# Kernel tuning notes

Measured on AMD Instinct MI355X. Metric: run time of the kernel, lower is better.

Reference implementation:

```python
import jax, jax.numpy as jnp
import numpy as np

DEPTH = 4
V = 4          # num_variables
B = 131072     # batch


def _level_counts(D, v):
    # n[d] = number of tree nodes whose depth attribute is d
    n = [0] * (D + 1)
    n[D] = 1
    for d in range(D, 1, -1):
        n[d - 1] = n[d] * (v + 1)   # v subformulas + 1 last_subformula
    n[0] = n[1]                      # each depth-1 node has exactly one depth-0 last
    return n


def setup_inputs() -> dict:
    key = jax.random.key(0)
    n = _level_counts(DEPTH, V)
    ks = jax.random.split(key, 2 * DEPTH + 2)
    inp = {"x": jax.random.uniform(ks[0], (B, V), jnp.float32, 0.5, 1.5)}
    # depth-0 constants (one per depth-0 node), like nn.Parameter(2*randn) but
    # scaled for numerical sanity of the deep product tree
    inp["lam0"] = jax.random.normal(ks[1], (n[0],), jnp.float32)
    for d in range(1, DEPTH + 1):
        inp[f"lam{d}"] = jax.random.normal(ks[2 * d], (n[d], V), jnp.float32)
        inp[f"pow{d}"] = 0.5 * jax.random.normal(ks[2 * d + 1], (n[d], V), jnp.float32)
    return inp


def reference(x, lam0, lam1, pow1, lam2, pow2, lam3, pow3, lam4, pow4):
    # Vectorized evaluation of the recursive tree, level by level.
    # Level d holds n_d independent NestedFormula nodes; each produces a (B,) vector.
    xt = x.T  # (V, B)
    batch = x.shape[0]
    # depth-0 nodes: constant lambda broadcast over batch
    f = jnp.broadcast_to(lam0[:, None], (lam0.shape[0], batch))  # (n0, B)
    lams = [lam1, lam2, lam3, lam4]
    pows = [pow1, pow2, pow3, pow4]
    for d in range(1, DEPTH + 1):
        lam, pw = lams[d - 1], pows[d - 1]           # (n_d, V)
        xp = xt[None, :, :] ** pw[:, :, None]        # (n_d, V, B): x_i ** power_i
        if d == 1:
            # subformula_result == 1; last subformula is the matching depth-0 node
            f = jnp.einsum('nv,nvb->nb', lam, xp) + f
        else:
            # children of node j at level d are nodes j*(V+1) .. j*(V+1)+V at level d-1:
            # first V are subformulas, last one is last_subformula
            fr = f.reshape(lam.shape[0], V + 1, batch)
            f = jnp.einsum('nv,nvb->nb', lam, xp * fr[:, :V, :]) + fr[:, V, :]
    return f[0][:, None]  # (B, 1)
```

## Files before the change

### kernel.cpp

```cpp
#include <hip/hip_runtime.h>


#define VV 4

__global__ __launch_bounds__(256) void nested_formula_kernel(
    const float4* __restrict__ x,
    const float*  __restrict__ lam0,
    const float*  __restrict__ lam1,
    const float*  __restrict__ pow1,
    const float*  __restrict__ lam2,
    const float*  __restrict__ pow2,
    const float*  __restrict__ lam3,
    const float*  __restrict__ pow3,
    const float*  __restrict__ lam4,
    const float*  __restrict__ pow4,
    float* __restrict__ out,
    int B)
{
    int b = blockIdx.x * blockDim.x + threadIdx.x;
    if (b >= B) return;

    float4 xv = x[b];
    float lx[VV] = { log2f(xv.x), log2f(xv.y), log2f(xv.z), log2f(xv.w) };

    float acc4 = 0.f, last4 = 0.f;
#pragma unroll
    for (int c3 = 0; c3 < VV + 1; ++c3) {
        float acc3 = 0.f, last3 = 0.f;
#pragma unroll
        for (int c2 = 0; c2 < VV + 1; ++c2) {
            int n2 = c3 * (VV + 1) + c2;
            float acc2 = 0.f, last2 = 0.f;
#pragma unroll
            for (int c1 = 0; c1 < VV + 1; ++c1) {
                int n1 = n2 * (VV + 1) + c1;
                float f1 = lam0[n1];
#pragma unroll
                for (int v = 0; v < VV; ++v) {
                    float xp = exp2f(pow1[n1 * VV + v] * lx[v]);
                    f1 = fmaf(lam1[n1 * VV + v], xp, f1);
                }
                if (c1 < VV) {
                    float xp = exp2f(pow2[n2 * VV + c1] * lx[c1]);
                    acc2 = fmaf(lam2[n2 * VV + c1] * xp, f1, acc2);
                } else {
                    last2 = f1;
                }
            }
            float f2 = acc2 + last2;
            if (c2 < VV) {
                float xp = exp2f(pow3[c3 * VV + c2] * lx[c2]);
                acc3 = fmaf(lam3[c3 * VV + c2] * xp, f2, acc3);
            } else {
                last3 = f2;
            }
        }
        float f3 = acc3 + last3;
        if (c3 < VV) {
            float xp = exp2f(pow4[c3] * lx[c3]);
            acc4 = fmaf(lam4[c3] * xp, f3, acc4);
        } else {
            last4 = f3;
        }
    }
    out[b] = acc4 + last4;
}

extern "C" void kernel_launch(void* const* d_in, const int* in_sizes, int n_in,
                              void* d_out, int out_size, void* d_ws, size_t ws_size,
                              hipStream_t stream) {
    const float4* x    = (const float4*)d_in[0];
    const float*  lam0 = (const float*)d_in[1];
    const float*  lam1 = (const float*)d_in[2];
    const float*  pow1 = (const float*)d_in[3];
    const float*  lam2 = (const float*)d_in[4];
    const float*  pow2 = (const float*)d_in[5];
    const float*  lam3 = (const float*)d_in[6];
    const float*  pow3 = (const float*)d_in[7];
    const float*  lam4 = (const float*)d_in[8];
    const float*  pow4 = (const float*)d_in[9];
    float* out = (float*)d_out;

    int B = in_sizes[0] / 4;
    int block = 256;
    int grid = (B + block - 1) / block;
    nested_formula_kernel<<<grid, block, 0, stream>>>(
        x, lam0, lam1, pow1, lam2, pow2, lam3, pow3, lam4, pow4, out, B);
}
```

Before: 95.92 us.

## Process four batch elements per thread and use raw hardware exp2/log intrinsics

Each thread now evaluates the formula tree for four batch elements, so every uniform load of the lam/pow parameters is reused across four elements, and the grid shrinks by four. The library log2f/exp2f calls are replaced by the AMDGPU hardware intrinsics, which skip denormal and range handling. This trades more registers per thread and fewer wavefronts for less scalar-load and instruction overhead, and accepts slightly different accuracy for edge-case inputs.

```diff
diff --git a/kernel.cpp b/kernel.cpp
--- a/kernel.cpp
+++ b/kernel.cpp
@@ -2,6 +2,7 @@
 
 
 #define VV 4
+#define E  4
 
 __global__ __launch_bounds__(256) void nested_formula_kernel(
     const float4* __restrict__ x,
@@ -17,53 +18,95 @@
     float* __restrict__ out,
     int B)
 {
-    int b = blockIdx.x * blockDim.x + threadIdx.x;
-    if (b >= B) return;
+    const int NT = gridDim.x * blockDim.x;
+    const int t  = blockIdx.x * blockDim.x + threadIdx.x;
 
-    float4 xv = x[b];
-    float lx[VV] = { log2f(xv.x), log2f(xv.y), log2f(xv.z), log2f(xv.w) };
+    float lx[E][VV];
+#pragma unroll
+    for (int e = 0; e < E; ++e) {
+        int b = t + e * NT;
+        float4 xv = (b < B) ? x[b] : make_float4(1.f, 1.f, 1.f, 1.f);
+        lx[e][0] = __builtin_amdgcn_logf(xv.x);
+        lx[e][1] = __builtin_amdgcn_logf(xv.y);
+        lx[e][2] = __builtin_amdgcn_logf(xv.z);
+        lx[e][3] = __builtin_amdgcn_logf(xv.w);
+    }
 
-    float acc4 = 0.f, last4 = 0.f;
+    float acc4[E], last4[E];
+#pragma unroll
+    for (int e = 0; e < E; ++e) { acc4[e] = 0.f; last4[e] = 0.f; }
+
 #pragma unroll
     for (int c3 = 0; c3 < VV + 1; ++c3) {
-        float acc3 = 0.f, last3 = 0.f;
+        float acc3[E], last3[E];
+#pragma unroll
+        for (int e = 0; e < E; ++e) { acc3[e] = 0.f; last3[e] = 0.f; }
+
 #pragma unroll
         for (int c2 = 0; c2 < VV + 1; ++c2) {
-            int n2 = c3 * (VV + 1) + c2;
-            float acc2 = 0.f, last2 = 0.f;
+            const int n2 = c3 * (VV + 1) + c2;
+            float acc2[E], last2[E];
+#pragma unroll
+            for (int e = 0; e < E; ++e) { acc2[e] = 0.f; last2[e] = 0.f; }
+
 #pragma unroll
             for (int c1 = 0; c1 < VV + 1; ++c1) {
-                int n1 = n2 * (VV + 1) + c1;
-                float f1 = lam0[n1];
+                const int n1 = n2 * (VV + 1) + c1;
+                float f1[E];
+                const float l0 = lam0[n1];
+#pragma unroll
+                for (int e = 0; e < E; ++e) f1[e] = l0;
 #pragma unroll
                 for (int v = 0; v < VV; ++v) {
-                    float xp = exp2f(pow1[n1 * VV + v] * lx[v]);
-                    f1 = fmaf(lam1[n1 * VV + v], xp, f1);
+                    const float p = pow1[n1 * VV + v];
+                    const float l = lam1[n1 * VV + v];
+#pragma unroll
+                    for (int e = 0; e < E; ++e)
+                        f1[e] = fmaf(l, __builtin_amdgcn_exp2f(p * lx[e][v]), f1[e]);
                 }
                 if (c1 < VV) {
-                    float xp = exp2f(pow2[n2 * VV + c1] * lx[c1]);
-                    acc2 = fmaf(lam2[n2 * VV + c1] * xp, f1, acc2);
+                    const float p = pow2[n2 * VV + c1];
+                    const float l = lam2[n2 * VV + c1];
+#pragma unroll
+                    for (int e = 0; e < E; ++e)
+                        acc2[e] = fmaf(l * __builtin_amdgcn_exp2f(p * lx[e][c1]), f1[e], acc2[e]);
                 } else {
-                    last2 = f1;
+#pragma unroll
+                    for (int e = 0; e < E; ++e) last2[e] = f1[e];
                 }
             }
-            float f2 = acc2 + last2;
+
             if (c2 < VV) {
-                float xp = exp2f(pow3[c3 * VV + c2] * lx[c2]);
-                acc3 = fmaf(lam3[c3 * VV + c2] * xp, f2, acc3);
+                const float p = pow3[c3 * VV + c2];
+                const float l = lam3[c3 * VV + c2];
+#pragma unroll
+                for (int e = 0; e < E; ++e)
+                    acc3[e] = fmaf(l * __builtin_amdgcn_exp2f(p * lx[e][c2]),
+                                   acc2[e] + last2[e], acc3[e]);
             } else {
-                last3 = f2;
+#pragma unroll
+                for (int e = 0; e < E; ++e) last3[e] = acc2[e] + last2[e];
             }
         }
-        float f3 = acc3 + last3;
+
         if (c3 < VV) {
-            float xp = exp2f(pow4[c3] * lx[c3]);
-            acc4 = fmaf(lam4[c3] * xp, f3, acc4);
+            const float p = pow4[c3];
+            const float l = lam4[c3];
+#pragma unroll
+            for (int e = 0; e < E; ++e)
+                acc4[e] = fmaf(l * __builtin_amdgcn_exp2f(p * lx[e][c3]),
+                               acc3[e] + last3[e], acc4[e]);
         } else {
-            last4 = f3;
+#pragma unroll
+            for (int e = 0; e < E; ++e) last4[e] = acc3[e] + last3[e];
         }
     }
-    out[b] = acc4 + last4;
+
+#pragma unroll
+    for (int e = 0; e < E; ++e) {
+        int b = t + e * NT;
+        if (b < B) out[b] = acc4[e] + last4[e];
+    }
 }
 
 extern "C" void kernel_launch(void* const* d_in, const int* in_sizes, int n_in,
@@ -83,7 +126,7 @@
 
     int B = in_sizes[0] / 4;
     int block = 256;
-    int grid = (B + block - 1) / block;
+    int grid = (B + block * E - 1) / (block * E);
     nested_formula_kernel<<<grid, block, 0, stream>>>(
         x, lam0, lam1, pow1, lam2, pow2, lam3, pow3, lam4, pow4, out, B);
 }
```

New measurement: 153.2 us. +59.7%, slower.

## Split formula tree across four grid rows and combine with atomic adds

Applied to the files above, without the earlier changes.

The grid gets a second dimension of four, and each row evaluates one slice of the depth-4 tree. The slices are the r-th depth-3 subtree, the r-th child of the last depth-3 node, and the r-th child of the innermost last chain. Partial results are summed into the output with atomics after a memset. Libm log2/exp2 are also replaced with the raw hardware intrinsics. This trades single-thread serial work for four times the threads plus memset and atomic traffic, and the per-row work is not evenly balanced.

```diff
diff --git a/kernel.cpp b/kernel.cpp
--- a/kernel.cpp
+++ b/kernel.cpp
@@ -3,7 +3,52 @@
 
 #define VV 4
 
-__global__ __launch_bounds__(256) void nested_formula_kernel(
+__device__ __forceinline__ float f1_eval(int n1, const float lx[VV],
+    const float* __restrict__ lam0, const float* __restrict__ lam1,
+    const float* __restrict__ pow1)
+{
+    float f = lam0[n1];
+#pragma unroll
+    for (int v = 0; v < VV; ++v)
+        f = fmaf(lam1[n1 * VV + v],
+                 __builtin_amdgcn_exp2f(pow1[n1 * VV + v] * lx[v]), f);
+    return f;
+}
+
+__device__ __forceinline__ float f2_eval(int n2, const float lx[VV],
+    const float* __restrict__ lam0, const float* __restrict__ lam1,
+    const float* __restrict__ pow1, const float* __restrict__ lam2,
+    const float* __restrict__ pow2)
+{
+    float acc = 0.f;
+#pragma unroll
+    for (int c1 = 0; c1 < VV; ++c1) {
+        float f1 = f1_eval(n2 * (VV + 1) + c1, lx, lam0, lam1, pow1);
+        acc = fmaf(lam2[n2 * VV + c1] *
+                       __builtin_amdgcn_exp2f(pow2[n2 * VV + c1] * lx[c1]),
+                   f1, acc);
+    }
+    return acc + f1_eval(n2 * (VV + 1) + VV, lx, lam0, lam1, pow1);
+}
+
+__device__ __forceinline__ float f3_eval(int n3, const float lx[VV],
+    const float* __restrict__ lam0, const float* __restrict__ lam1,
+    const float* __restrict__ pow1, const float* __restrict__ lam2,
+    const float* __restrict__ pow2, const float* __restrict__ lam3,
+    const float* __restrict__ pow3)
+{
+    float acc = 0.f;
+#pragma unroll
+    for (int c2 = 0; c2 < VV; ++c2) {
+        float f2 = f2_eval(n3 * (VV + 1) + c2, lx, lam0, lam1, pow1, lam2, pow2);
+        acc = fmaf(lam3[n3 * VV + c2] *
+                       __builtin_amdgcn_exp2f(pow3[n3 * VV + c2] * lx[c2]),
+                   f2, acc);
+    }
+    return acc + f2_eval(n3 * (VV + 1) + VV, lx, lam0, lam1, pow1, lam2, pow2);
+}
+
+__global__ __launch_bounds__(256) void nested_formula_r4(
     const float4* __restrict__ x,
     const float*  __restrict__ lam0,
     const float*  __restrict__ lam1,
@@ -17,53 +62,30 @@
     float* __restrict__ out,
     int B)
 {
-    int b = blockIdx.x * blockDim.x + threadIdx.x;
+    const int r = blockIdx.y;
+    const int b = blockIdx.x * blockDim.x + threadIdx.x;
     if (b >= B) return;
 
     float4 xv = x[b];
-    float lx[VV] = { log2f(xv.x), log2f(xv.y), log2f(xv.z), log2f(xv.w) };
+    float lx[VV] = { __builtin_amdgcn_logf(xv.x), __builtin_amdgcn_logf(xv.y),
+                     __builtin_amdgcn_logf(xv.z), __builtin_amdgcn_logf(xv.w) };
+    const float lxr = (r == 0) ? lx[0] : (r == 1) ? lx[1] : (r == 2) ? lx[2] : lx[3];
 
-    float acc4 = 0.f, last4 = 0.f;
-#pragma unroll
-    for (int c3 = 0; c3 < VV + 1; ++c3) {
-        float acc3 = 0.f, last3 = 0.f;
-#pragma unroll
-        for (int c2 = 0; c2 < VV + 1; ++c2) {
-            int n2 = c3 * (VV + 1) + c2;
-            float acc2 = 0.f, last2 = 0.f;
-#pragma unroll
-            for (int c1 = 0; c1 < VV + 1; ++c1) {
-                int n1 = n2 * (VV + 1) + c1;
-                float f1 = lam0[n1];
-#pragma unroll
-                for (int v = 0; v < VV; ++v) {
-                    float xp = exp2f(pow1[n1 * VV + v] * lx[v]);
-                    f1 = fmaf(lam1[n1 * VV + v], xp, f1);
-                }
-                if (c1 < VV) {
-                    float xp = exp2f(pow2[n2 * VV + c1] * lx[c1]);
-                    acc2 = fmaf(lam2[n2 * VV + c1] * xp, f1, acc2);
-                } else {
-                    last2 = f1;
-                }
-            }
-            float f2 = acc2 + last2;
-            if (c2 < VV) {
-                float xp = exp2f(pow3[c3 * VV + c2] * lx[c2]);
-                acc3 = fmaf(lam3[c3 * VV + c2] * xp, f2, acc3);
-            } else {
-                last3 = f2;
-            }
-        }
-        float f3 = acc3 + last3;
-        if (c3 < VV) {
-            float xp = exp2f(pow4[c3] * lx[c3]);
-            acc4 = fmaf(lam4[c3] * xp, f3, acc4);
-        } else {
-            last4 = f3;
-        }
-    }
-    out[b] = acc4 + last4;
+    float f3 = f3_eval(r, lx, lam0, lam1, pow1, lam2, pow2, lam3, pow3);
+    float partial = lam4[r] * __builtin_amdgcn_exp2f(pow4[r] * lxr) * f3;
+
+    float f2 = f2_eval(4 * (VV + 1) + r, lx, lam0, lam1, pow1, lam2, pow2);
+    partial = fmaf(lam3[4 * VV + r] * __builtin_amdgcn_exp2f(pow3[4 * VV + r] * lxr),
+                   f2, partial);
+
+    float f1 = f1_eval(24 * (VV + 1) + r, lx, lam0, lam1, pow1);
+    partial = fmaf(lam2[24 * VV + r] * __builtin_amdgcn_exp2f(pow2[24 * VV + r] * lxr),
+                   f1, partial);
+
+    if (r == 0)
+        partial += f1_eval(24 * (VV + 1) + VV, lx, lam0, lam1, pow1);
+
+    unsafeAtomicAdd(&out[b], partial);
 }
 
 extern "C" void kernel_launch(void* const* d_in, const int* in_sizes, int n_in,
@@ -82,8 +104,10 @@
     float* out = (float*)d_out;
 
     int B = in_sizes[0] / 4;
-    int block = 256;
-    int grid = (B + block - 1) / block;
-    nested_formula_kernel<<<grid, block, 0, stream>>>(
+    hipMemsetAsync(out, 0, (size_t)B * sizeof(float), stream);
+
+    dim3 block(256, 1, 1);
+    dim3 grid((B + 255) / 256, 4, 1);
+    nested_formula_r4<<<grid, block, 0, stream>>>(
         x, lam0, lam1, pow1, lam2, pow2, lam3, pow3, lam4, pow4, out, B);
 }
```

Result: faster. 88.82 us (-7.4%).

## Split tree top level across wavefronts with two samples per thread and LDS reduction

Applied to the files above, without the earlier changes.

Each block now covers 128 samples with 5 wavefronts. Each wavefront evaluates one of the five depth-3 subtrees for two samples per lane, and the results are combined through shared memory. Each thread also shares parameter loads between its two samples and uses raw hardware exp2/log intrinsics instead of the library versions. The goal is to cut serial work per thread, amortize the uniform parameter loads, and drop denormal/range handling overhead. The cost is a __syncthreads barrier, LDS traffic, and possible precision differences from the raw intrinsics.

```diff
diff --git a/kernel.cpp b/kernel.cpp
--- a/kernel.cpp
+++ b/kernel.cpp
@@ -3,7 +3,67 @@
 
 #define VV 4
 
-__global__ __launch_bounds__(256) void nested_formula_kernel(
+__device__ __forceinline__ void f1_eval2(int n1,
+    const float lxA[VV], const float lxB[VV],
+    const float* __restrict__ lam0, const float* __restrict__ lam1,
+    const float* __restrict__ pow1, float& fA, float& fB)
+{
+    float a = lam0[n1], b = a;
+#pragma unroll
+    for (int v = 0; v < VV; ++v) {
+        const float p = pow1[n1 * VV + v];
+        const float l = lam1[n1 * VV + v];
+        a = fmaf(l, __builtin_amdgcn_exp2f(p * lxA[v]), a);
+        b = fmaf(l, __builtin_amdgcn_exp2f(p * lxB[v]), b);
+    }
+    fA = a; fB = b;
+}
+
+__device__ __forceinline__ void f2_eval2(int n2,
+    const float lxA[VV], const float lxB[VV],
+    const float* __restrict__ lam0, const float* __restrict__ lam1,
+    const float* __restrict__ pow1, const float* __restrict__ lam2,
+    const float* __restrict__ pow2, float& fA, float& fB)
+{
+    float accA = 0.f, accB = 0.f;
+#pragma unroll
+    for (int c1 = 0; c1 < VV; ++c1) {
+        float f1A, f1B;
+        f1_eval2(n2 * (VV + 1) + c1, lxA, lxB, lam0, lam1, pow1, f1A, f1B);
+        const float l = lam2[n2 * VV + c1];
+        const float p = pow2[n2 * VV + c1];
+        accA = fmaf(l * __builtin_amdgcn_exp2f(p * lxA[c1]), f1A, accA);
+        accB = fmaf(l * __builtin_amdgcn_exp2f(p * lxB[c1]), f1B, accB);
+    }
+    float lA, lB;
+    f1_eval2(n2 * (VV + 1) + VV, lxA, lxB, lam0, lam1, pow1, lA, lB);
+    fA = accA + lA; fB = accB + lB;
+}
+
+__device__ __forceinline__ void f3_eval2(int n3,
+    const float lxA[VV], const float lxB[VV],
+    const float* __restrict__ lam0, const float* __restrict__ lam1,
+    const float* __restrict__ pow1, const float* __restrict__ lam2,
+    const float* __restrict__ pow2, const float* __restrict__ lam3,
+    const float* __restrict__ pow3, float& fA, float& fB)
+{
+    float accA = 0.f, accB = 0.f;
+#pragma unroll
+    for (int c2 = 0; c2 < VV; ++c2) {
+        float f2A, f2B;
+        f2_eval2(n3 * (VV + 1) + c2, lxA, lxB, lam0, lam1, pow1, lam2, pow2,
+                 f2A, f2B);
+        const float l = lam3[n3 * VV + c2];
+        const float p = pow3[n3 * VV + c2];
+        accA = fmaf(l * __builtin_amdgcn_exp2f(p * lxA[c2]), f2A, accA);
+        accB = fmaf(l * __builtin_amdgcn_exp2f(p * lxB[c2]), f2B, accB);
+    }
+    float lA, lB;
+    f2_eval2(n3 * (VV + 1) + VV, lxA, lxB, lam0, lam1, pow1, lam2, pow2, lA, lB);
+    fA = accA + lA; fB = accB + lB;
+}
+
+__global__ __launch_bounds__(320) void nested_formula_r7(
     const float4* __restrict__ x,
     const float*  __restrict__ lam0,
     const float*  __restrict__ lam1,
@@ -17,53 +77,50 @@
     float* __restrict__ out,
     int B)
 {
-    int b = blockIdx.x * blockDim.x + threadIdx.x;
-    if (b >= B) return;
+    const int lane = threadIdx.x & 63;
+    const int r    = threadIdx.x >> 6;
+    const int b0   = blockIdx.x * 128 + lane;
+    const int b1   = b0 + 64;
 
-    float4 xv = x[b];
-    float lx[VV] = { log2f(xv.x), log2f(xv.y), log2f(xv.z), log2f(xv.w) };
+    __shared__ float red[5][128];
 
-    float acc4 = 0.f, last4 = 0.f;
-#pragma unroll
-    for (int c3 = 0; c3 < VV + 1; ++c3) {
-        float acc3 = 0.f, last3 = 0.f;
-#pragma unroll
-        for (int c2 = 0; c2 < VV + 1; ++c2) {
-            int n2 = c3 * (VV + 1) + c2;
-            float acc2 = 0.f, last2 = 0.f;
-#pragma unroll
-            for (int c1 = 0; c1 < VV + 1; ++c1) {
-                int n1 = n2 * (VV + 1) + c1;
-                float f1 = lam0[n1];
-#pragma unroll
-                for (int v = 0; v < VV; ++v) {
-                    float xp = exp2f(pow1[n1 * VV + v] * lx[v]);
-                    f1 = fmaf(lam1[n1 * VV + v], xp, f1);
-                }
-                if (c1 < VV) {
-                    float xp = exp2f(pow2[n2 * VV + c1] * lx[c1]);
-                    acc2 = fmaf(lam2[n2 * VV + c1] * xp, f1, acc2);
-                } else {
-                    last2 = f1;
-                }
-            }
-            float f2 = acc2 + last2;
-            if (c2 < VV) {
-                float xp = exp2f(pow3[c3 * VV + c2] * lx[c2]);
-                acc3 = fmaf(lam3[c3 * VV + c2] * xp, f2, acc3);
-            } else {
-                last3 = f2;
-            }
-        }
-        float f3 = acc3 + last3;
-        if (c3 < VV) {
-            float xp = exp2f(pow4[c3] * lx[c3]);
-            acc4 = fmaf(lam4[c3] * xp, f3, acc4);
-        } else {
-            last4 = f3;
-        }
+    const float4 xa = x[min(b0, B - 1)];
+    const float4 xb = x[min(b1, B - 1)];
+    const float lxA[VV] = { __builtin_amdgcn_logf(xa.x), __builtin_amdgcn_logf(xa.y),
+                            __builtin_amdgcn_logf(xa.z), __builtin_amdgcn_logf(xa.w) };
+    const float lxB[VV] = { __builtin_amdgcn_logf(xb.x), __builtin_amdgcn_logf(xb.y),
+                            __builtin_amdgcn_logf(xb.z), __builtin_amdgcn_logf(xb.w) };
+
+    float f3A, f3B;
+    f3_eval2(r, lxA, lxB, lam0, lam1, pow1, lam2, pow2, lam3, pow3, f3A, f3B);
+
+    float pA, pB;
+    if (r < 4) {
+        const float l4 = lam4[r];
+        const float p4 = pow4[r];
+        const float lxrA = (r == 0) ? lxA[0] : (r == 1) ? lxA[1]
+                         : (r == 2) ? lxA[2] : lxA[3];
+        const float lxrB = (r == 0) ? lxB[0] : (r == 1) ? lxB[1]
+                         : (r == 2) ? lxB[2] : lxB[3];
+        pA = l4 * __builtin_amdgcn_exp2f(p4 * lxrA) * f3A;
+        pB = l4 * __builtin_amdgcn_exp2f(p4 * lxrB) * f3B;
+    } else {
+        pA = f3A;
+        pB = f3B;
     }
-    out[b] = acc4 + last4;
+
+    red[r][lane]      = pA;
+    red[r][lane + 64] = pB;
+    __syncthreads();
+
+    if (r == 0) {
+        float sA = ((red[0][lane] + red[1][lane]) +
+                    (red[2][lane] + red[3][lane])) + red[4][lane];
+        float sB = ((red[0][lane + 64] + red[1][lane + 64]) +
+                    (red[2][lane + 64] + red[3][lane + 64])) + red[4][lane + 64];
+        if (b0 < B) out[b0] = sA;
+        if (b1 < B) out[b1] = sB;
+    }
 }
 
 extern "C" void kernel_launch(void* const* d_in, const int* in_sizes, int n_in,
@@ -82,8 +139,8 @@
     float* out = (float*)d_out;
 
     int B = in_sizes[0] / 4;
-    int block = 256;
-    int grid = (B + block - 1) / block;
-    nested_formula_kernel<<<grid, block, 0, stream>>>(
+    dim3 block(320, 1, 1);
+    dim3 grid((B + 127) / 128, 1, 1);
+    nested_formula_r7<<<grid, block, 0, stream>>>(
         x, lam0, lam1, pow1, lam2, pow2, lam3, pow3, lam4, pow4, out, B);
 }
```

Result: faster. 82.63 us (-13.9%).
